# Optimization experiments

Measured on AMD Instinct MI355X. Metric: run time of the kernel, lower is better.

Reference implementation:

```python
import jax, jax.numpy as jnp
import numpy as np

B, L, D, H = 2, 2048, 2048, 16
DH = D // H

def setup_inputs() -> dict:
    key = jax.random.key(0)
    ks = jax.random.split(key, 7)
    q = jax.random.normal(ks[0], (B, L, D), dtype=jnp.float32)
    k = jax.random.normal(ks[1], (B, L, D), dtype=jnp.float32)
    v = jax.random.normal(ks[2], (B, L, D), dtype=jnp.float32)
    # causal mask: True means masked (matches torch masked_fill semantics)
    attn_mask = jnp.triu(jnp.ones((L, L), dtype=bool), k=1)[None, None, :, :]
    scale = 0.02
    wq = jax.random.normal(ks[3], (D, D), dtype=jnp.float32) * scale
    wk = jax.random.normal(ks[4], (D, D), dtype=jnp.float32) * scale
    wv = jax.random.normal(ks[5], (D, D), dtype=jnp.float32) * scale
    wo = jax.random.normal(ks[6], (D, D), dtype=jnp.float32) * scale
    return {"q": q, "k": k, "v": v, "attn_mask": attn_mask,
            "wq": wq, "wk": wk, "wv": wv, "wo": wo}

def _split_heads(x):
    b, l, _ = x.shape
    return x.reshape(b, l, H, DH).transpose(0, 2, 1, 3)  # [B,H,L,DH]

def reference(q, k, v, attn_mask, wq, wk, wv, wo):
    # torch Linear: y = x @ W.T (bias=False)
    qh = _split_heads(q @ wq.T)
    kh = _split_heads(k @ wk.T)
    vh = _split_heads(v @ wv.T)
    scale = 1.0 / np.sqrt(DH).astype(np.float32)
    scores = jnp.einsum('bhqd,bhkd->bhqk', qh, kh) * scale
    neg = jnp.finfo(scores.dtype).min
    scores = jnp.where(attn_mask, neg, scores)
    attn = jax.nn.softmax(scores, axis=-1)
    ctx = jnp.einsum('bhqk,bhkd->bhqd', attn, vh)
    ctx = ctx.transpose(0, 2, 1, 3).reshape(q.shape[0], q.shape[1], D)
    return ctx @ wo.T
```

## Files before the change

kernel.cpp:

```cpp
#include <hip/hip_runtime.h>

#define B_  2
#define L_  2048
#define D_  2048
#define H_  16
#define DH_ 128
#define K_  2048

typedef __attribute__((ext_vector_type(8))) short bf16x8;
typedef __attribute__((ext_vector_type(4))) float f32x4;
typedef __attribute__((ext_vector_type(4))) float float4v;
typedef __attribute__((ext_vector_type(8))) unsigned short u16x8;
typedef __attribute__((ext_vector_type(4))) unsigned short u16x4;

__device__ __forceinline__ unsigned short f2bf(float f) {
  unsigned u = __builtin_bit_cast(unsigned, f);
  u += 0x7fffu + ((u >> 16) & 1u);
  return (unsigned short)(u >> 16);
}

typedef __attribute__((address_space(3))) unsigned int lds_uint;
typedef __attribute__((address_space(1))) const unsigned int glob_uint;
__device__ __forceinline__ void gld16(const void* g, void* l) {
  __builtin_amdgcn_global_load_lds((glob_uint*)g, (lds_uint*)l, 16, 0, 0);
}

#define BAR() do { asm volatile("" ::: "memory"); __builtin_amdgcn_s_barrier(); asm volatile("" ::: "memory"); } while (0)
#define VMCNT(n) asm volatile("s_waitcnt vmcnt(" #n ")" ::: "memory")

__global__ void cvt_all(const float* __restrict__ wq, const float* __restrict__ wk,
                        const float* __restrict__ wv, const float* __restrict__ wo,
                        const float* __restrict__ q, const float* __restrict__ k,
                        const float* __restrict__ v, unsigned short* __restrict__ ws,
                        int nacts) {
  const size_t DD = (size_t)D_ * D_;
  const size_t BLD = (size_t)B_ * L_ * D_;
  const int z = blockIdx.z;
  const float* src;
  unsigned short* dst;
  size_t nelem;
  if (z < 4) {
    src = (z == 0) ? wq : (z == 1) ? wk : (z == 2) ? wv : wo;
    dst = ws + (size_t)z * DD;
    nelem = DD;
  } else {
    if (z - 4 >= nacts) return;
    src = (z == 4) ? q : (z == 5) ? k : v;
    dst = ws + 4 * DD + (size_t)(z - 4) * BLD;
    nelem = BLD;
  }
  size_t i = ((size_t)blockIdx.x * 256 + threadIdx.x) * 8;
  if (i >= nelem) return;
  float4v x0 = *(const float4v*)(src + i);
  float4v x1 = *(const float4v*)(src + i + 4);
  u16x8 p;
  p[0]=f2bf(x0[0]); p[1]=f2bf(x0[1]); p[2]=f2bf(x0[2]); p[3]=f2bf(x0[3]);
  p[4]=f2bf(x1[0]); p[5]=f2bf(x1[1]); p[6]=f2bf(x1[2]); p[7]=f2bf(x1[3]);
  *(u16x8*)(dst + i) = p;
}

template <int KIND>
__global__ __launch_bounds__(512, 2) void gemm8(
    const unsigned short* __restrict__ a0, const unsigned short* __restrict__ a1,
    const unsigned short* __restrict__ a2,
    const unsigned short* __restrict__ w0, const unsigned short* __restrict__ w1,
    const unsigned short* __restrict__ w2,
    unsigned short* __restrict__ Qh, unsigned short* __restrict__ Kh,
    unsigned short* __restrict__ Vt, float* __restrict__ OF) {
  __shared__ unsigned short smem[3 * 24576];

  const int lin = blockIdx.x + 32 * (blockIdx.y + 8 * blockIdx.z);
  const int cpx = KIND ? 32 : 96;
  const int s = (lin & 7) * cpx + (lin >> 3);
  const int mt = s & 31;
  const int r_ = s >> 5;
  const int ntile = KIND ? r_ : (r_ & 7);
  const int z = KIND ? 0 : (r_ >> 3);

  const unsigned short* A = KIND ? a0 : (z == 0 ? a0 : z == 1 ? a1 : a2);
  const unsigned short* W = KIND ? w0 : (z == 0 ? w0 : z == 1 ? w1 : w2);
  const int mode = KIND ? 2 : (z == 2 ? 1 : 0);

  const int bm0 = mt * 128;
  const int bn0 = ntile * 256;

  const int tid = threadIdx.x;
  const int wid = tid >> 6, lane = tid & 63;
  const int wr = wid >> 2, wc = wid & 3;
  const int l15 = lane & 15, l4 = lane >> 4;

  const unsigned short* gsrc[6];
  int ldst[6];
  {
#pragma unroll
    for (int i = 0; i < 2; ++i) {
      const int c = i * 512 + tid, r = c >> 3, s0 = c & 7;
      gsrc[i] = A + (size_t)(bm0 + r) * K_ + ((s0 ^ (r & 7)) << 3);
      ldst[i] = c * 8;
    }
#pragma unroll
    for (int u = 0; u < 2; ++u)
#pragma unroll
      for (int i = 0; i < 2; ++i) {
        const int c = i * 512 + tid, r = c >> 3, s0 = c & 7;
        gsrc[2 + u * 2 + i] = W + (size_t)(bn0 + u * 128 + r) * K_ + ((s0 ^ (r & 7)) << 3);
        ldst[2 + u * 2 + i] = 8192 + (u * 1024 + c) * 8;
      }
  }
#define STAGE(idx, p) do { gld16(gsrc[idx], &smem[(p) * 24576 + ldst[idx]]); gsrc[idx] += 64; } while (0)

  int offA[2][2][2], offB[4][2];
#pragma unroll
  for (int mh = 0; mh < 2; ++mh)
#pragma unroll
    for (int ml = 0; ml < 2; ++ml)
#pragma unroll
      for (int ks = 0; ks < 2; ++ks) {
        const int row = wr * 64 + mh * 32 + ml * 16 + l15;
        const int ch = ks * 4 + l4;
        offA[mh][ml][ks] = row * 64 + ((ch ^ (row & 7)) << 3);
      }
#pragma unroll
  for (int nf = 0; nf < 4; ++nf)
#pragma unroll
    for (int ks = 0; ks < 2; ++ks) {
      const int rowb = wc * 64 + nf * 16 + l15;
      const int ch = ks * 4 + l4;
      offB[nf][ks] = 8192 + rowb * 64 + ((ch ^ (rowb & 7)) << 3);
    }

  f32x4 acc[4][4];
#pragma unroll
  for (int m = 0; m < 4; ++m)
#pragma unroll
    for (int n = 0; n < 4; ++n) { f32x4 zz = {0.f, 0.f, 0.f, 0.f}; acc[m][n] = zz; }

  STAGE(0, 0); STAGE(1, 0); STAGE(2, 0); STAGE(3, 0); STAGE(4, 0); STAGE(5, 0);
  STAGE(0, 1); STAGE(1, 1); STAGE(2, 1); STAGE(3, 1); STAGE(4, 1); STAGE(5, 1);
  VMCNT(6);
  BAR();

  int p = 0;
  for (int t = 0; t < 32; ++t) {
    int p2 = p + 2; if (p2 >= 3) p2 -= 3;
    const unsigned short* bA = &smem[p * 24576];
    bf16x8 af[2][2], bfr[4][2];
#pragma unroll
    for (int ml = 0; ml < 2; ++ml)
#pragma unroll
      for (int ks = 0; ks < 2; ++ks)
        af[ml][ks] = *(const bf16x8*)&bA[offA[0][ml][ks]];
#pragma unroll
    for (int nf = 0; nf < 4; ++nf)
#pragma unroll
      for (int ks = 0; ks < 2; ++ks)
        bfr[nf][ks] = *(const bf16x8*)&bA[offB[nf][ks]];
    if (t < 30) { STAGE(0, p2); STAGE(1, p2); STAGE(2, p2); STAGE(3, p2); }
    BAR();
    __builtin_amdgcn_s_setprio(1);
#pragma unroll
    for (int ml = 0; ml < 2; ++ml)
#pragma unroll
      for (int nf = 0; nf < 4; ++nf)
#pragma unroll
        for (int ks = 0; ks < 2; ++ks)
          acc[ml][nf] = __builtin_amdgcn_mfma_f32_16x16x32_bf16(af[ml][ks], bfr[nf][ks], acc[ml][nf], 0, 0, 0);
    __builtin_amdgcn_s_setprio(0);
    BAR();
#pragma unroll
    for (int ml = 0; ml < 2; ++ml)
#pragma unroll
      for (int ks = 0; ks < 2; ++ks)
        af[ml][ks] = *(const bf16x8*)&bA[offA[1][ml][ks]];
    if (t < 30) { STAGE(4, p2); STAGE(5, p2); }
    BAR();
    __builtin_amdgcn_s_setprio(1);
#pragma unroll
    for (int ml = 0; ml < 2; ++ml)
#pragma unroll
      for (int nf = 0; nf < 4; ++nf)
#pragma unroll
        for (int ks = 0; ks < 2; ++ks)
          acc[2 + ml][nf] = __builtin_amdgcn_mfma_f32_16x16x32_bf16(af[ml][ks], bfr[nf][ks], acc[2 + ml][nf], 0, 0, 0);
    __builtin_amdgcn_s_setprio(0);
    if (t < 30) { VMCNT(6); } else { VMCNT(0); }
    BAR();
    p = (p == 2) ? 0 : p + 1;
  }
#undef STAGE

  if (mode == 0) {
    unsigned short* O = (z == 0) ? Qh : Kh;
#pragma unroll
    for (int mf = 0; mf < 4; ++mf) {
      const int rr = bm0 + wr * 64 + mf * 16 + l4 * 4;
#pragma unroll
      for (int nf = 0; nf < 4; ++nf) {
        const int cc = bn0 + wc * 64 + nf * 16 + l15;
        const int h = cc >> 7, dh = cc & 127;
#pragma unroll
        for (int j = 0; j < 4; ++j) {
          const int r2 = rr + j;
          O[((size_t)((r2 >> 11) * H_ + h) * L_ + (r2 & 2047)) * DH_ + dh] = f2bf(acc[mf][nf][j]);
        }
      }
    }
  } else if (mode == 1) {
    unsigned short* T = smem;
#pragma unroll
    for (int mf = 0; mf < 4; ++mf) {
      const int rl = wr * 64 + mf * 16 + l4 * 4;
#pragma unroll
      for (int nf = 0; nf < 4; ++nf) {
        const int cl = wc * 64 + nf * 16 + l15;
        u16x4 vv;
#pragma unroll
        for (int j = 0; j < 4; ++j) vv[j] = f2bf(acc[mf][nf][j]);
        *(u16x4*)&T[cl * 128 + (((rl >> 3) ^ (cl & 7)) << 3) + (rl & 7)] = vv;
      }
    }
    __syncthreads();
    const int b = bm0 >> 11, lbase = bm0 & 2047;
#pragma unroll
    for (int it = 0; it < 8; ++it) {
      const int idx = it * 512 + tid;
      const int rT = idx >> 4, sT = idx & 15;
      u16x8 val = *(const u16x8*)&T[rT * 128 + ((sT ^ (rT & 7)) << 3)];
      const int n = bn0 + rT, h = n >> 7, dh = n & 127;
      *(u16x8*)&Vt[((size_t)(b * H_ + h) * DH_ + dh) * L_ + lbase + sT * 8] = val;
    }
  } else {
#pragma unroll
    for (int mf = 0; mf < 4; ++mf) {
      const int rr = bm0 + wr * 64 + mf * 16 + l4 * 4;
#pragma unroll
      for (int nf = 0; nf < 4; ++nf) {
        const int cc = bn0 + wc * 64 + nf * 16 + l15;
#pragma unroll
        for (int j = 0; j < 4; ++j) OF[(size_t)(rr + j) * D_ + cc] = acc[mf][nf][j];
      }
    }
  }
}

__global__ __launch_bounds__(256, 2) void proj_gemm_f32a(
    const float* __restrict__ q, const float* __restrict__ k, const float* __restrict__ v,
    const unsigned short* __restrict__ wqb, const unsigned short* __restrict__ wkb,
    const unsigned short* __restrict__ wvb,
    unsigned short* __restrict__ Qh, unsigned short* __restrict__ Kh,
    unsigned short* __restrict__ Vt) {
  __shared__ unsigned short smem[128 * 136];
  unsigned short* As = smem;
  unsigned short* Bs = smem + 128 * 64;

  const int z = blockIdx.z;
  const float* A = (z == 0) ? q : (z == 1) ? k : v;
  const unsigned short* W = (z == 0) ? wqb : (z == 1) ? wkb : wvb;

  const int tid = threadIdx.x;
  const int wave = tid >> 6, lane = tid & 63;
  const int wr = wave >> 1, wc = wave & 1;
  const int bm0 = blockIdx.x * 128;
  const int bn0 = blockIdx.y * 128;
  const int l15 = lane & 15, l4 = lane >> 4;

  f32x4 acc[4][4];
#pragma unroll
  for (int m = 0; m < 4; m++)
#pragma unroll
    for (int n = 0; n < 4; n++) { f32x4 zz = {0.f, 0.f, 0.f, 0.f}; acc[m][n] = zz; }

  for (int k0 = 0; k0 < K_; k0 += 64) {
#pragma unroll
    for (int it = 0; it < 4; ++it) {
      const int base = it * 256 + wave * 64;
      const int ch = base + lane;
      const int r = ch >> 3, c = ch & 7;
      gld16(W + (size_t)(bn0 + r) * K_ + (k0 + c * 8), Bs + base * 8);
    }
#pragma unroll
    for (int it = 0; it < 4; ++it) {
      const int ch = it * 256 + tid;
      const int r = ch >> 3, c = ch & 7;
      const float* g = A + (size_t)(bm0 + r) * K_ + (k0 + c * 8);
      float4v x0 = *(const float4v*)g;
      float4v x1 = *(const float4v*)(g + 4);
      u16x8 pp;
      pp[0]=f2bf(x0[0]); pp[1]=f2bf(x0[1]); pp[2]=f2bf(x0[2]); pp[3]=f2bf(x0[3]);
      pp[4]=f2bf(x1[0]); pp[5]=f2bf(x1[1]); pp[6]=f2bf(x1[2]); pp[7]=f2bf(x1[3]);
      *(u16x8*)&As[ch * 8] = pp;
    }
    __syncthreads();
#pragma unroll
    for (int ks = 0; ks < 2; ++ks) {
      const int kc = ks * 32 + l4 * 8;
      bf16x8 af[4], bfr[4];
#pragma unroll
      for (int m = 0; m < 4; m++) af[m] = *(const bf16x8*)&As[(wr * 64 + m * 16 + l15) * 64 + kc];
#pragma unroll
      for (int n = 0; n < 4; n++) bfr[n] = *(const bf16x8*)&Bs[(wc * 64 + n * 16 + l15) * 64 + kc];
#pragma unroll
      for (int m = 0; m < 4; m++)
#pragma unroll
        for (int n = 0; n < 4; n++)
          acc[m][n] = __builtin_amdgcn_mfma_f32_16x16x32_bf16(af[m], bfr[n], acc[m][n], 0, 0, 0);
    }
    __syncthreads();
  }

  if (z < 2) {
    unsigned short* O = (z == 0) ? Qh : Kh;
#pragma unroll
    for (int m = 0; m < 4; m++) {
      const int rr = bm0 + wr * 64 + m * 16 + l4 * 4;
#pragma unroll
      for (int n = 0; n < 4; n++) {
        const int cc = bn0 + wc * 64 + n * 16 + l15;
        const int h = cc >> 7, dh = cc & 127;
#pragma unroll
        for (int j = 0; j < 4; j++) {
          const int r2 = rr + j;
          O[((size_t)((r2 >> 11) * H_ + h) * L_ + (r2 & 2047)) * DH_ + dh] = f2bf(acc[m][n][j]);
        }
      }
    }
  } else {
    __syncthreads();
    unsigned short* T = smem;
#pragma unroll
    for (int m = 0; m < 4; m++)
#pragma unroll
      for (int n = 0; n < 4; n++) {
        const int cl = wc * 64 + n * 16 + l15;
        const int rl = wr * 64 + m * 16 + l4 * 4;
#pragma unroll
        for (int j = 0; j < 4; j++) T[cl * 136 + rl + j] = f2bf(acc[m][n][j]);
      }
    __syncthreads();
    const int b = bm0 >> 11, lbase = bm0 & 2047;
    const int hb = bn0 >> 7;
#pragma unroll
    for (int it = 0; it < 8; ++it) {
      const int idx = it * 256 + tid;
      const int dhl = idx >> 4, c = idx & 15;
      u16x8 val = *(const u16x8*)&T[dhl * 136 + c * 8];
      *(u16x8*)&Vt[((size_t)(b * H_ + hb) * DH_ + dhl) * L_ + lbase + c * 8] = val;
    }
  }
}

#define SCALE_ 0.08838834764831845f

__global__ __launch_bounds__(256, 2) void attn_kernel(
    const unsigned short* __restrict__ Qh, const unsigned short* __restrict__ Kh,
    const unsigned short* __restrict__ Vt, unsigned short* __restrict__ ctx) {
  __shared__ unsigned short Ks[128 * 128];
  __shared__ unsigned short Vs[128 * 128];
  __shared__ unsigned short Ps[4][16 * 128];

  const int pair = blockIdx.x, bh = blockIdx.y;
  const size_t hoff = (size_t)bh * L_ * DH_;
  const unsigned short* Qp = Qh + hoff;
  const unsigned short* Kp = Kh + hoff;
  const unsigned short* Vp = Vt + hoff;

  const int tid = threadIdx.x, wave = tid >> 6, lane = tid & 63;
  const int l15 = lane & 15, l4 = lane >> 4;
  const int b = bh >> 4, h = bh & 15;

#pragma unroll 1
  for (int p = 0; p < 2; ++p) {
    const int qt = p ? (31 - pair) : pair;
    const int ntiles = (qt + 2) >> 1;

    bf16x8 qf[4];
    {
      const int qrow = qt * 64 + wave * 16 + l15;
#pragma unroll
      for (int s = 0; s < 4; s++)
        qf[s] = *(const bf16x8*)&Qp[(size_t)qrow * DH_ + s * 32 + l4 * 8];
    }

    f32x4 o[8];
#pragma unroll
    for (int df = 0; df < 8; df++) { f32x4 zz = {0.f, 0.f, 0.f, 0.f}; o[df] = zz; }
    float m_r[4] = {-1e30f, -1e30f, -1e30f, -1e30f};
    float l_r[4] = {0.f, 0.f, 0.f, 0.f};

    for (int kt = 0; kt < ntiles; ++kt) {
#pragma unroll
      for (int it = 0; it < 8; ++it) {
        const int base = it * 256 + wave * 64;
        const int ch = base + lane;
        const int r = ch >> 4, s = ch & 15;
        gld16(Kp + (size_t)(kt * 128 + r) * DH_ + ((s ^ (r & 7)) * 8), (unsigned short*)Ks + base * 8);
      }
#pragma unroll
      for (int it = 0; it < 8; ++it) {
        const int base = it * 256 + wave * 64;
        const int ch = base + lane;
        const int r = ch >> 4, s = ch & 15;
        gld16(Vp + (size_t)r * L_ + kt * 128 + ((s ^ (r & 7)) * 8), (unsigned short*)Vs + base * 8);
      }
      __syncthreads();

      f32x4 sa[8];
#pragma unroll
      for (int f = 0; f < 8; f++) { f32x4 zz = {0.f, 0.f, 0.f, 0.f}; sa[f] = zz; }
      __builtin_amdgcn_s_setprio(1);
#pragma unroll
      for (int ks = 0; ks < 4; ++ks) {
        const int c = ks * 4 + l4;
#pragma unroll
        for (int f = 0; f < 8; ++f) {
          const int n = f * 16 + l15;
          bf16x8 kf = *(const bf16x8*)&Ks[n * 128 + ((c ^ (n & 7)) * 8)];
          sa[f] = __builtin_amdgcn_mfma_f32_16x16x32_bf16(qf[ks], kf, sa[f], 0, 0, 0);
        }
      }
      __builtin_amdgcn_s_setprio(0);

      const bool last = (kt == ntiles - 1);
#pragma unroll
      for (int f = 0; f < 8; f++) {
        const int kg = kt * 128 + f * 16 + l15;
#pragma unroll
        for (int j = 0; j < 4; j++) {
          float t = sa[f][j] * SCALE_;
          if (last && kg > qt * 64 + wave * 16 + l4 * 4 + j) t = -1e30f;
          sa[f][j] = t;
        }
      }

#pragma unroll
      for (int j = 0; j < 4; j++) {
        float mx = fmaxf(fmaxf(fmaxf(sa[0][j], sa[1][j]), fmaxf(sa[2][j], sa[3][j])),
                         fmaxf(fmaxf(sa[4][j], sa[5][j]), fmaxf(sa[6][j], sa[7][j])));
#pragma unroll
        for (int d = 1; d < 16; d <<= 1) mx = fmaxf(mx, __shfl_xor(mx, d));
        const float mnew = fmaxf(m_r[j], mx);
        const float alpha = __expf(m_r[j] - mnew);
        float rs = 0.f;
        const int row = l4 * 4 + j;
#pragma unroll
        for (int f = 0; f < 8; f++) {
          float pp = __expf(sa[f][j] - mnew);
          rs += pp;
          const int col = f * 16 + l15;
          const int c = col >> 3;
          Ps[wave][row * 128 + ((c ^ (row & 7)) * 8) + (col & 7)] = f2bf(pp);
        }
#pragma unroll
        for (int d = 1; d < 16; d <<= 1) rs += __shfl_xor(rs, d);
        l_r[j] = l_r[j] * alpha + rs;
        m_r[j] = mnew;
#pragma unroll
        for (int df = 0; df < 8; df++) o[df][j] *= alpha;
      }

      __builtin_amdgcn_s_setprio(1);
#pragma unroll
      for (int ksl = 0; ksl < 4; ++ksl) {
        const int pc = ksl * 4 + l4;
        bf16x8 pf = *(const bf16x8*)&Ps[wave][l15 * 128 + ((pc ^ (l15 & 7)) * 8)];
#pragma unroll
        for (int df = 0; df < 8; ++df) {
          const int vr = df * 16 + l15;
          bf16x8 vf = *(const bf16x8*)&Vs[vr * 128 + ((pc ^ (vr & 7)) * 8)];
          o[df] = __builtin_amdgcn_mfma_f32_16x16x32_bf16(pf, vf, o[df], 0, 0, 0);
        }
      }
      __builtin_amdgcn_s_setprio(0);
      __syncthreads();
    }

#pragma unroll
    for (int j = 0; j < 4; j++) {
      const float inv = 1.0f / l_r[j];
      const int lq = qt * 64 + wave * 16 + l4 * 4 + j;
      const size_t rowb = ((size_t)(b * L_ + lq)) * D_ + h * DH_;
#pragma unroll
      for (int df = 0; df < 8; ++df)
        ctx[rowb + df * 16 + l15] = f2bf(o[df][j] * inv);
    }
  }
}

extern "C" void kernel_launch(void* const* d_in, const int* in_sizes, int n_in,
                              void* d_out, int out_size, void* d_ws, size_t ws_size,
                              hipStream_t stream) {
  const float* q  = (const float*)d_in[0];
  const float* k  = (const float*)d_in[1];
  const float* v  = (const float*)d_in[2];
  const float* wq = (const float*)d_in[4];
  const float* wk = (const float*)d_in[5];
  const float* wv = (const float*)d_in[6];
  const float* wo = (const float*)d_in[7];

  const size_t DD = (size_t)D_ * D_;
  const size_t BLD = (size_t)B_ * L_ * D_;
  unsigned short* ws  = (unsigned short*)d_ws;
  unsigned short* wqb = ws;
  unsigned short* wkb = wqb + DD;
  unsigned short* wvb = wkb + DD;
  unsigned short* wob = wvb + DD;

  const size_t need_full = (4 * DD + 7 * BLD) * 2;

  if (ws_size >= need_full) {
    unsigned short* qb  = wob + DD;
    unsigned short* kb  = qb + BLD;
    unsigned short* vb  = kb + BLD;
    unsigned short* QhP = vb + BLD;
    unsigned short* KhP = QhP + BLD;
    unsigned short* VtP = KhP + BLD;
    unsigned short* ctx = VtP + BLD;

    cvt_all<<<dim3(4096, 1, 7), 256, 0, stream>>>(wq, wk, wv, wo, q, k, v, ws, 3);
    gemm8<0><<<dim3(32, 8, 3), 512, 0, stream>>>(qb, kb, vb, wqb, wkb, wvb, QhP, KhP, VtP, nullptr);
    attn_kernel<<<dim3(16, 32), 256, 0, stream>>>(QhP, KhP, VtP, ctx);
    gemm8<1><<<dim3(32, 8, 1), 512, 0, stream>>>(ctx, nullptr, nullptr, wob, nullptr, nullptr,
                                                 nullptr, nullptr, nullptr, (float*)d_out);
  } else {
    unsigned short* QhP = wob + DD;
    unsigned short* KhP = QhP + BLD;
    unsigned short* VtP = KhP + BLD;
    unsigned short* ctx = VtP + BLD;

    cvt_all<<<dim3(4096, 1, 4), 256, 0, stream>>>(wq, wk, wv, wo, q, k, v, ws, 0);
    proj_gemm_f32a<<<dim3(32, 16, 3), 256, 0, stream>>>(q, k, v, wqb, wkb, wvb, QhP, KhP, VtP);
    attn_kernel<<<dim3(16, 32), 256, 0, stream>>>(QhP, KhP, VtP, ctx);
    gemm8<1><<<dim3(32, 8, 1), 512, 0, stream>>>(ctx, nullptr, nullptr, wob, nullptr, nullptr,
                                                 nullptr, nullptr, nullptr, (float*)d_out);
  }
}
```

Before: 291.3 us.

## Split K across warp pairs in GEMM with LDS reduction of partial accumulators

Reorganizes the 8 warps of the bf16 GEMM so pairs of warps split each 64-wide K slice (each takes one 32-wide half), while each warp covers a 64x128 output tile instead of 64x64. Each warp now loads 4 A fragments and 8 B fragments per stage rather than 4 A and 8 B across two K steps, reducing redundant LDS fragment reads per MFMA. At the end, the odd warps write their fp32 partial sums to LDS and the even warps add them and perform the epilogue. This doubles accumulator registers per warp (128 floats) and adds an LDS reduction and extra barrier, risking register pressure, lower occupancy, and half the warps idling in the epilogue.

```diff
diff --git a/kernel.cpp b/kernel.cpp
--- a/kernel.cpp
+++ b/kernel.cpp
@@ -86,7 +86,9 @@
 
   const int tid = threadIdx.x;
   const int wid = tid >> 6, lane = tid & 63;
-  const int wr = wid >> 2, wc = wid & 3;
+  const int kw = wid & 1;
+  const int wc = (wid >> 1) & 1;
+  const int wr = wid >> 2;
   const int l15 = lane & 15, l4 = lane >> 4;
 
   const unsigned short* gsrc[6];
@@ -109,31 +111,26 @@
   }
 #define STAGE(idx, p) do { gld16(gsrc[idx], &smem[(p) * 24576 + ldst[idx]]); gsrc[idx] += 64; } while (0)
 
-  int offA[2][2][2], offB[4][2];
-#pragma unroll
-  for (int mh = 0; mh < 2; ++mh)
-#pragma unroll
-    for (int ml = 0; ml < 2; ++ml)
-#pragma unroll
-      for (int ks = 0; ks < 2; ++ks) {
-        const int row = wr * 64 + mh * 32 + ml * 16 + l15;
-        const int ch = ks * 4 + l4;
-        offA[mh][ml][ks] = row * 64 + ((ch ^ (row & 7)) << 3);
-      }
-#pragma unroll
-  for (int nf = 0; nf < 4; ++nf)
-#pragma unroll
-    for (int ks = 0; ks < 2; ++ks) {
-      const int rowb = wc * 64 + nf * 16 + l15;
-      const int ch = ks * 4 + l4;
-      offB[nf][ks] = 8192 + rowb * 64 + ((ch ^ (rowb & 7)) << 3);
-    }
-
-  f32x4 acc[4][4];
+  int offA[4], offB[8];
+  {
+    const int ch = kw * 4 + l4;
+#pragma unroll
+    for (int mf = 0; mf < 4; ++mf) {
+      const int row = wr * 64 + mf * 16 + l15;
+      offA[mf] = row * 64 + ((ch ^ (row & 7)) << 3);
+    }
+#pragma unroll
+    for (int nf = 0; nf < 8; ++nf) {
+      const int rowb = wc * 128 + nf * 16 + l15;
+      offB[nf] = 8192 + rowb * 64 + ((ch ^ (rowb & 7)) << 3);
+    }
+  }
+
+  f32x4 acc[4][8];
 #pragma unroll
   for (int m = 0; m < 4; ++m)
 #pragma unroll
-    for (int n = 0; n < 4; ++n) { f32x4 zz = {0.f, 0.f, 0.f, 0.f}; acc[m][n] = zz; }
+    for (int n = 0; n < 8; ++n) { f32x4 zz = {0.f, 0.f, 0.f, 0.f}; acc[m][n] = zz; }
 
   STAGE(0, 0); STAGE(1, 0); STAGE(2, 0); STAGE(3, 0); STAGE(4, 0); STAGE(5, 0);
   STAGE(0, 1); STAGE(1, 1); STAGE(2, 1); STAGE(3, 1); STAGE(4, 1); STAGE(5, 1);
@@ -144,44 +141,31 @@
   for (int t = 0; t < 32; ++t) {
     int p2 = p + 2; if (p2 >= 3) p2 -= 3;
     const unsigned short* bA = &smem[p * 24576];
-    bf16x8 af[2][2], bfr[4][2];
-#pragma unroll
-    for (int ml = 0; ml < 2; ++ml)
-#pragma unroll
-      for (int ks = 0; ks < 2; ++ks)
-        af[ml][ks] = *(const bf16x8*)&bA[offA[0][ml][ks]];
-#pragma unroll
-    for (int nf = 0; nf < 4; ++nf)
-#pragma unroll
-      for (int ks = 0; ks < 2; ++ks)
-        bfr[nf][ks] = *(const bf16x8*)&bA[offB[nf][ks]];
+    bf16x8 af[4], bfr[4];
+#pragma unroll
+    for (int mf = 0; mf < 4; ++mf) af[mf] = *(const bf16x8*)&bA[offA[mf]];
+#pragma unroll
+    for (int nf = 0; nf < 4; ++nf) bfr[nf] = *(const bf16x8*)&bA[offB[nf]];
     if (t < 30) { STAGE(0, p2); STAGE(1, p2); STAGE(2, p2); STAGE(3, p2); }
     BAR();
     __builtin_amdgcn_s_setprio(1);
 #pragma unroll
-    for (int ml = 0; ml < 2; ++ml)
+    for (int mf = 0; mf < 4; ++mf)
 #pragma unroll
       for (int nf = 0; nf < 4; ++nf)
-#pragma unroll
-        for (int ks = 0; ks < 2; ++ks)
-          acc[ml][nf] = __builtin_amdgcn_mfma_f32_16x16x32_bf16(af[ml][ks], bfr[nf][ks], acc[ml][nf], 0, 0, 0);
+        acc[mf][nf] = __builtin_amdgcn_mfma_f32_16x16x32_bf16(af[mf], bfr[nf], acc[mf][nf], 0, 0, 0);
     __builtin_amdgcn_s_setprio(0);
     BAR();
 #pragma unroll
-    for (int ml = 0; ml < 2; ++ml)
-#pragma unroll
-      for (int ks = 0; ks < 2; ++ks)
-        af[ml][ks] = *(const bf16x8*)&bA[offA[1][ml][ks]];
+    for (int nf = 0; nf < 4; ++nf) bfr[nf] = *(const bf16x8*)&bA[offB[4 + nf]];
     if (t < 30) { STAGE(4, p2); STAGE(5, p2); }
     BAR();
     __builtin_amdgcn_s_setprio(1);
 #pragma unroll
-    for (int ml = 0; ml < 2; ++ml)
+    for (int mf = 0; mf < 4; ++mf)
 #pragma unroll
       for (int nf = 0; nf < 4; ++nf)
-#pragma unroll
-        for (int ks = 0; ks < 2; ++ks)
-          acc[2 + ml][nf] = __builtin_amdgcn_mfma_f32_16x16x32_bf16(af[ml][ks], bfr[nf][ks], acc[2 + ml][nf], 0, 0, 0);
+        acc[mf][4 + nf] = __builtin_amdgcn_mfma_f32_16x16x32_bf16(af[mf], bfr[nf], acc[mf][4 + nf], 0, 0, 0);
     __builtin_amdgcn_s_setprio(0);
     if (t < 30) { VMCNT(6); } else { VMCNT(0); }
     BAR();
@@ -189,34 +173,61 @@
   }
 #undef STAGE
 
+  float* R = (float*)smem;
+  const int rbase = (wr * 2 + wc) * (64 * 128);
+  if (kw) {
+#pragma unroll
+    for (int mf = 0; mf < 4; ++mf)
+#pragma unroll
+      for (int nf = 0; nf < 8; ++nf)
+#pragma unroll
+        for (int j = 0; j < 4; ++j)
+          R[rbase + (mf * 16 + l4 * 4 + j) * 128 + nf * 16 + l15] = acc[mf][nf][j];
+  }
+  __syncthreads();
+  if (!kw) {
+#pragma unroll
+    for (int mf = 0; mf < 4; ++mf)
+#pragma unroll
+      for (int nf = 0; nf < 8; ++nf)
+#pragma unroll
+        for (int j = 0; j < 4; ++j)
+          acc[mf][nf][j] += R[rbase + (mf * 16 + l4 * 4 + j) * 128 + nf * 16 + l15];
+  }
+
   if (mode == 0) {
-    unsigned short* O = (z == 0) ? Qh : Kh;
-#pragma unroll
-    for (int mf = 0; mf < 4; ++mf) {
-      const int rr = bm0 + wr * 64 + mf * 16 + l4 * 4;
-#pragma unroll
-      for (int nf = 0; nf < 4; ++nf) {
-        const int cc = bn0 + wc * 64 + nf * 16 + l15;
-        const int h = cc >> 7, dh = cc & 127;
-#pragma unroll
-        for (int j = 0; j < 4; ++j) {
-          const int r2 = rr + j;
-          O[((size_t)((r2 >> 11) * H_ + h) * L_ + (r2 & 2047)) * DH_ + dh] = f2bf(acc[mf][nf][j]);
+    if (!kw) {
+      unsigned short* O = (z == 0) ? Qh : Kh;
+#pragma unroll
+      for (int mf = 0; mf < 4; ++mf) {
+        const int rr = bm0 + wr * 64 + mf * 16 + l4 * 4;
+#pragma unroll
+        for (int nf = 0; nf < 8; ++nf) {
+          const int cc = bn0 + wc * 128 + nf * 16 + l15;
+          const int h = cc >> 7, dh = cc & 127;
+#pragma unroll
+          for (int j = 0; j < 4; ++j) {
+            const int r2 = rr + j;
+            O[((size_t)((r2 >> 11) * H_ + h) * L_ + (r2 & 2047)) * DH_ + dh] = f2bf(acc[mf][nf][j]);
+          }
         }
       }
     }
   } else if (mode == 1) {
+    __syncthreads();
     unsigned short* T = smem;
-#pragma unroll
-    for (int mf = 0; mf < 4; ++mf) {
-      const int rl = wr * 64 + mf * 16 + l4 * 4;
-#pragma unroll
-      for (int nf = 0; nf < 4; ++nf) {
-        const int cl = wc * 64 + nf * 16 + l15;
-        u16x4 vv;
-#pragma unroll
-        for (int j = 0; j < 4; ++j) vv[j] = f2bf(acc[mf][nf][j]);
-        *(u16x4*)&T[cl * 128 + (((rl >> 3) ^ (cl & 7)) << 3) + (rl & 7)] = vv;
+    if (!kw) {
+#pragma unroll
+      for (int mf = 0; mf < 4; ++mf) {
+        const int rl = wr * 64 + mf * 16 + l4 * 4;
+#pragma unroll
+        for (int nf = 0; nf < 8; ++nf) {
+          const int cl = wc * 128 + nf * 16 + l15;
+          u16x4 vv;
+#pragma unroll
+          for (int j = 0; j < 4; ++j) vv[j] = f2bf(acc[mf][nf][j]);
+          *(u16x4*)&T[cl * 136 + rl] = vv;
+        }
       }
     }
     __syncthreads();
@@ -224,20 +235,22 @@
 #pragma unroll
     for (int it = 0; it < 8; ++it) {
       const int idx = it * 512 + tid;
-      const int rT = idx >> 4, sT = idx & 15;
-      u16x8 val = *(const u16x8*)&T[rT * 128 + ((sT ^ (rT & 7)) << 3)];
+      const int rT = idx >> 4, cT = idx & 15;
+      u16x8 val = *(const u16x8*)&T[rT * 136 + cT * 8];
       const int n = bn0 + rT, h = n >> 7, dh = n & 127;
-      *(u16x8*)&Vt[((size_t)(b * H_ + h) * DH_ + dh) * L_ + lbase + sT * 8] = val;
+      *(u16x8*)&Vt[((size_t)(b * H_ + h) * DH_ + dh) * L_ + lbase + cT * 8] = val;
     }
   } else {
-#pragma unroll
-    for (int mf = 0; mf < 4; ++mf) {
-      const int rr = bm0 + wr * 64 + mf * 16 + l4 * 4;
-#pragma unroll
-      for (int nf = 0; nf < 4; ++nf) {
-        const int cc = bn0 + wc * 64 + nf * 16 + l15;
-#pragma unroll
-        for (int j = 0; j < 4; ++j) OF[(size_t)(rr + j) * D_ + cc] = acc[mf][nf][j];
+    if (!kw) {
+#pragma unroll
+      for (int mf = 0; mf < 4; ++mf) {
+        const int rr = bm0 + wr * 64 + mf * 16 + l4 * 4;
+#pragma unroll
+        for (int nf = 0; nf < 8; ++nf) {
+          const int cc = bn0 + wc * 128 + nf * 16 + l15;
+#pragma unroll
+          for (int j = 0; j < 4; ++j) OF[(size_t)(rr + j) * D_ + cc] = acc[mf][nf][j];
+        }
       }
     }
   }
```

Measured after the change: 295.9 us. Within noise of the previous version (+1.6%).
